# Optimization experiments

Hardware: AMD Instinct MI355X
Metric: run time of the kernel (lower is better)

Reference implementation:

```python
import jax, jax.numpy as jnp
import numpy as np

# Model constants (match init_kwargs)
DIM = 1024
INTER = 1024
E = 32          # n_routed_experts
K = 4           # n_activated_experts
G = 8           # n_expert_groups
LG = 4          # n_limited_groups
ROUTE_SCALE = 1.0
CAP_FACTOR = 1.25
B, S = 4, 2048


def setup_inputs() -> dict:
    key = jax.random.key(0)
    ks = jax.random.split(key, 9)
    sd = DIM ** -0.5
    si = INTER ** -0.5
    x = jax.random.normal(ks[0], (B, S, DIM), jnp.float32)
    wg = jax.random.normal(ks[1], (E, DIM), jnp.float32) * sd          # gate weight [E, dim]
    w1 = jax.random.normal(ks[2], (E, DIM, INTER), jnp.float32) * sd   # stacked expert w1
    w3 = jax.random.normal(ks[3], (E, DIM, INTER), jnp.float32) * sd   # stacked expert w3
    w2 = jax.random.normal(ks[4], (E, INTER, DIM), jnp.float32) * si   # stacked expert w2
    sw1 = jax.random.normal(ks[5], (DIM, INTER), jnp.float32) * sd     # shared SwiGLU
    sw3 = jax.random.normal(ks[6], (DIM, INTER), jnp.float32) * sd
    sw2 = jax.random.normal(ks[7], (INTER, DIM), jnp.float32) * si
    return dict(x=x, wg=wg, w1=w1, w2=w2, w3=w3, sw1=sw1, sw2=sw2, sw3=sw3)


def _gate(xf, wg):
    # Group-limited top-k gating (router_noise_std=0, temperature=1.0).
    logits = xf @ wg.T                                  # [N, E]
    scores = jax.nn.softmax(logits, axis=-1)
    sg = scores.reshape(-1, G, E // G)                  # [N, G, E/G]
    group_scores = sg.max(axis=-1)                      # [N, G]
    _, gtop = jax.lax.top_k(group_scores, LG)           # [N, LG]
    keep_g = jnp.sum(jax.nn.one_hot(gtop, G, dtype=jnp.float32), axis=1) > 0  # [N, G]
    masked = jnp.where(keep_g[:, :, None], sg, -jnp.inf).reshape(-1, E)
    _, idx = jax.lax.top_k(masked, K)                   # [N, K]
    w = jnp.take_along_axis(scores, idx, axis=1)        # gather from ORIGINAL scores
    w = w / (w.sum(-1, keepdims=True) + 1e-9) * ROUTE_SCALE
    return w.astype(xf.dtype), idx


def _forward(x, wg, w1, w2, w3, sw1, sw2, sw3):
    shape = x.shape
    xf = x.reshape(-1, DIM)
    N = xf.shape[0]
    cap = max(1, int(CAP_FACTOR * N * K / E))           # per-expert capacity (static)
    w, idx = _gate(xf, wg)

    # --- dispatch with capacity: position of each (token, slot) within its expert,
    # counted in row-major (token-major) order == torch.where order in the original.
    fe = idx.reshape(-1)                                # [N*K] expert ids
    oh = jax.nn.one_hot(fe, E, dtype=jnp.int32)         # [N*K, E]
    pos = (jnp.cumsum(oh, axis=0) * oh).sum(-1) - 1     # rank within expert
    keep = pos < cap
    dest = jnp.where(keep, fe * cap + pos, E * cap)     # dropped -> pad slot
    tok = jnp.arange(N * K, dtype=jnp.int32) // K
    buf_tok = jnp.full((E * cap + 1,), N, jnp.int32).at[dest].set(tok)[:-1]       # [E*cap]
    buf_w = jnp.zeros((E * cap + 1,), x.dtype).at[dest].set(w.reshape(-1))[:-1]   # [E*cap]

    # --- grouped gather-GEMM-scatter (pad row of zeros for empty slots)
    xp = jnp.concatenate([xf, jnp.zeros((1, DIM), x.dtype)], axis=0)
    xe = xp[buf_tok].reshape(E, cap, DIM)
    h = jax.nn.silu(jnp.einsum('ecd,edh->ech', xe, w1)) * jnp.einsum('ecd,edh->ech', xe, w3)
    out = jnp.einsum('ech,ehd->ecd', h, w2) * buf_w.reshape(E, cap, 1)
    y = jnp.zeros((N + 1, DIM), x.dtype).at[buf_tok].add(out.reshape(E * cap, DIM))[:N]

    # --- shared experts (SwiGLU with inter dim == inter_dim via expansion formula)
    z = (jax.nn.silu(xf @ sw1) * (xf @ sw3)) @ sw2
    return (y + z).reshape(shape)


def reference(x, wg, w1, w2, w3, sw1, sw2, sw3):
    return _forward(x, wg, w1, w2, w3, sw1, sw2, sw3)
```

## Files before the change

### kernel.cpp

```cpp
#include <hip/hip_runtime.h>
#include <stdint.h>

#define NTOK 8192
#define CAP  1280
#define NEXP 32

typedef __bf16 bf16x8 __attribute__((ext_vector_type(8)));
typedef float f32x4 __attribute__((ext_vector_type(4)));
typedef unsigned short u16;

__device__ __forceinline__ u16 f2bf(float f) {
  unsigned u = __builtin_bit_cast(unsigned, f);
  u = (u + 0x7fffu + ((u >> 16) & 1u)) >> 16;
  return (u16)u;
}
__device__ __forceinline__ float bf2f(u16 h) {
  return __builtin_bit_cast(float, ((unsigned)h) << 16);
}

__device__ __forceinline__ void gload16(const void* g, void* l) {
  __builtin_amdgcn_global_load_lds(
      (const __attribute__((address_space(1))) void*)g,
      (__attribute__((address_space(3))) void*)l, 16, 0, 0);
}

__global__ __launch_bounds__(256) void conv_x_kernel(const float* __restrict__ in,
                                                     u16* __restrict__ out) {
  int i = blockIdx.x * 256 + threadIdx.x;
  float4 v = reinterpret_cast<const float4*>(in)[i];
  uint2 o;
  o.x = (unsigned)f2bf(v.x) | ((unsigned)f2bf(v.y) << 16);
  o.y = (unsigned)f2bf(v.z) | ((unsigned)f2bf(v.w) << 16);
  reinterpret_cast<uint2*>(out)[i] = o;
}

__global__ __launch_bounds__(256) void tconv_all_kernel(
    const float* __restrict__ w1, const float* __restrict__ w3,
    const float* __restrict__ w2, const float* __restrict__ sw1,
    const float* __restrict__ sw3, const float* __restrict__ sw2,
    u16* __restrict__ w1t, u16* __restrict__ w3t, u16* __restrict__ w2t,
    u16* __restrict__ sw1t, u16* __restrict__ sw3t, u16* __restrict__ sw2t) {
  __shared__ float tile[32][33];
  const int z = blockIdx.z;
  const float* src;
  u16* dst;
  if (z < 32)      { src = w1 + (size_t)z * 1048576;        dst = w1t + (size_t)z * 1048576; }
  else if (z < 64) { src = w3 + (size_t)(z - 32) * 1048576; dst = w3t + (size_t)(z - 32) * 1048576; }
  else if (z < 96) { src = w2 + (size_t)(z - 64) * 1048576; dst = w2t + (size_t)(z - 64) * 1048576; }
  else if (z == 96){ src = sw1; dst = sw1t; }
  else if (z == 97){ src = sw3; dst = sw3t; }
  else             { src = sw2; dst = sw2t; }
  int r0 = blockIdx.x * 32, c0 = blockIdx.y * 32;
  int tid = threadIdx.x;
#pragma unroll
  for (int i = 0; i < 4; ++i) {
    int t = tid + i * 256, r = t >> 5, c = t & 31;
    tile[r][c] = src[(size_t)(r0 + r) * 1024 + (c0 + c)];
  }
  __syncthreads();
#pragma unroll
  for (int i = 0; i < 4; ++i) {
    int t = tid + i * 256, cc = t >> 5, rr = t & 31;
    dst[(size_t)(c0 + cc) * 1024 + (r0 + rr)] = f2bf(tile[rr][cc]);
  }
}

__global__ __launch_bounds__(256) void gate_kernel(const float* __restrict__ x,
                                                   const float* __restrict__ wg,
                                                   int* __restrict__ gidx,
                                                   float* __restrict__ gw) {
  const int t = blockIdx.x;
  __shared__ float xl[1024];
  __shared__ float logits[32];
  const int tid = threadIdx.x;
  reinterpret_cast<float4*>(xl)[tid] = reinterpret_cast<const float4*>(x + (size_t)t * 1024)[tid];
  __syncthreads();
  const int e = tid >> 3, p = tid & 7;
  const float4* wrow = reinterpret_cast<const float4*>(wg + (size_t)e * 1024);
  const float4* xv4 = reinterpret_cast<const float4*>(xl);
  float s = 0.f;
#pragma unroll
  for (int i = 0; i < 32; ++i) {
    int c = p + 8 * i;
    float4 xv = xv4[c];
    float4 wv = wrow[c];
    s += xv.x * wv.x + xv.y * wv.y + xv.z * wv.z + xv.w * wv.w;
  }
  s += __shfl_xor(s, 1);
  s += __shfl_xor(s, 2);
  s += __shfl_xor(s, 4);
  if (p == 0) logits[e] = s;
  __syncthreads();
  if (tid == 0) {
    float m = logits[0];
#pragma unroll
    for (int i = 1; i < 32; ++i) m = fmaxf(m, logits[i]);
    float sum = 0.f;
#pragma unroll
    for (int i = 0; i < 32; ++i) sum += expf(logits[i] - m);
    float gm[8];
#pragma unroll
    for (int g = 0; g < 8; ++g) {
      float v = logits[4 * g];
      v = fmaxf(v, logits[4 * g + 1]);
      v = fmaxf(v, logits[4 * g + 2]);
      v = fmaxf(v, logits[4 * g + 3]);
      gm[g] = v;
    }
    unsigned gkeep = 0;
    for (int it = 0; it < 4; ++it) {
      float best = -3.4e38f; int bg = 0;
#pragma unroll
      for (int g = 0; g < 8; ++g) {
        bool ok = !((gkeep >> g) & 1u);
        if (ok && gm[g] > best) { best = gm[g]; bg = g; }
      }
      gkeep |= 1u << bg;
    }
    unsigned allow = 0;
#pragma unroll
    for (int g = 0; g < 8; ++g)
      if ((gkeep >> g) & 1u) allow |= 0xFu << (4 * g);
    unsigned taken = 0;
    float wsum = 0.f;
    int ids[4]; float wv[4];
    for (int sIt = 0; sIt < 4; ++sIt) {
      float best = -3.4e38f; int be = 0;
#pragma unroll
      for (int i = 0; i < 32; ++i) {
        bool ok = ((allow >> i) & 1u) && !((taken >> i) & 1u);
        float v = logits[i];
        if (ok && v > best) { best = v; be = i; }
      }
      taken |= 1u << be;
      ids[sIt] = be;
      float wq = expf(logits[be] - m) / sum;
      wv[sIt] = wq;
      wsum += wq;
    }
    float inv = 1.f / (wsum + 1e-9f);
#pragma unroll
    for (int sIt = 0; sIt < 4; ++sIt) {
      gidx[t * 4 + sIt] = ids[sIt];
      gw[t * 4 + sIt] = wv[sIt] * inv;
    }
  }
}

__global__ __launch_bounds__(256) void initbuf_kernel(int* __restrict__ bt, float* __restrict__ bw) {
  int i = blockIdx.x * 256 + threadIdx.x;
  if (i < NEXP * CAP) { bt[i] = -1; bw[i] = 0.f; }
}

__global__ __launch_bounds__(1024) void rank_kernel(const int* __restrict__ gidx,
                                                    const float* __restrict__ gw,
                                                    int* __restrict__ buf_tok,
                                                    float* __restrict__ buf_w,
                                                    int* __restrict__ cnt,
                                                    int* __restrict__ tslot) {
  const int e = blockIdx.x;
  const int tid = threadIdx.x, wid = tid >> 6, lane = tid & 63;
  __shared__ int wtot[16];
  int base = 0;
  for (int j0 = 0; j0 < NTOK * 4; j0 += 1024) {
    int j = j0 + tid;
    bool match = (gidx[j] == e);
    unsigned long long mb = __ballot(match);
    if (lane == 0) wtot[wid] = __popcll(mb);
    __syncthreads();
    int woff = 0, btot = 0;
#pragma unroll
    for (int w = 0; w < 16; ++w) {
      int c = wtot[w];
      if (w < wid) woff += c;
      btot += c;
    }
    if (match) {
      int pos = base + woff + __popcll(mb & ((1ull << lane) - 1ull));
      if (pos < CAP) {
        buf_tok[e * CAP + pos] = j >> 2;
        buf_w[e * CAP + pos] = gw[j];
        tslot[j] = e * CAP + pos;
      } else {
        tslot[j] = -1;
      }
    }
    base += btot;
    __syncthreads();
  }
  if (tid == 0) cnt[e] = (base < CAP) ? base : CAP;
}

#define UP_PHASE(M, EXTRA, LAST)                                                                  \
  {                                                                                               \
    bf16x8 a0 = afrag(cur, M, 0);                                                                 \
    bf16x8 a1 = afrag(cur, M, 1);                                                                 \
    EXTRA                                                                                         \
    __builtin_amdgcn_s_barrier();                                                                 \
    __builtin_amdgcn_s_setprio(1);                                                                \
    _Pragma("unroll")                                                                             \
    for (int n = 0; n < 4; ++n) {                                                                 \
      acc1[M][n] = __builtin_amdgcn_mfma_f32_16x16x32_bf16(a0, b1f[n][0], acc1[M][n], 0, 0, 0);   \
      acc1[M][n] = __builtin_amdgcn_mfma_f32_16x16x32_bf16(a1, b1f[n][1], acc1[M][n], 0, 0, 0);   \
      acc3[M][n] = __builtin_amdgcn_mfma_f32_16x16x32_bf16(a0, b3f[n][0], acc3[M][n], 0, 0, 0);   \
      acc3[M][n] = __builtin_amdgcn_mfma_f32_16x16x32_bf16(a1, b3f[n][1], acc3[M][n], 0, 0, 0);   \
    }                                                                                             \
    __builtin_amdgcn_s_setprio(0);                                                                \
    LAST                                                                                          \
    __builtin_amdgcn_s_barrier();                                                                 \
  }

__global__ __launch_bounds__(512) void up8_kernel(const u16* __restrict__ X,
                                                  const u16* __restrict__ w1t,
                                                  const u16* __restrict__ w3t,
                                                  const u16* __restrict__ sw1t,
                                                  const u16* __restrict__ sw3t,
                                                  u16* __restrict__ hs,
                                                  u16* __restrict__ he,
                                                  const int* __restrict__ btok,
                                                  const int* __restrict__ cnt) {
  extern __shared__ __align__(16) u16 lds_raw[];
  const int tid = threadIdx.x, wid = tid >> 6, lane = tid & 63;
  const int bid = blockIdx.x;
  const int xcd = bid & 7, off = bid >> 3;
  bool expert;
  int mt, nt, e = 0;
  const u16 *B1, *B3;
  u16* H;
  if (off < 160) {
    expert = true;
    int id = xcd * 160 + off;
    e = id / 40;
    int r = id % 40;
    mt = r % 5;
    nt = r / 5;
    if (mt * 256 >= cnt[e]) return;
    B1 = w1t + ((size_t)e << 20);
    B3 = w3t + ((size_t)e << 20);
    H = he + (size_t)(e * CAP + mt * 256) * 1024;
  } else {
    expert = false;
    int id = xcd * 32 + (off - 160);
    mt = id % 32;
    nt = id / 32;
    B1 = sw1t;
    B3 = sw3t;
    H = hs + (size_t)mt * 256 * 1024;
  }
  const int wr = wid >> 1, wc = wid & 1;
  const int fr = lane & 15, fw = lane >> 4;

  const int srow = wid * 8 + (lane >> 3);
  const int swin = (((lane & 7) ^ (srow & 7)) << 3);

  const u16* aP[4];
#pragma unroll
  for (int j = 0; j < 4; ++j) {
    int row = mt * 256 + j * 64 + srow;
    int grow;
    if (expert) {
      int t0 = btok[e * CAP + row];
      grow = (t0 < 0) ? 0 : t0;
    } else {
      grow = row;
    }
    aP[j] = X + (size_t)grow * 1024 + swin;
  }
  const u16* b1P[2];
  const u16* b3P[2];
#pragma unroll
  for (int j = 0; j < 2; ++j) {
    int row = nt * 128 + j * 64 + srow;
    b1P[j] = B1 + (size_t)row * 1024 + swin;
    b3P[j] = B3 + (size_t)row * 1024 + swin;
  }

  auto ldsA  = [&](int b) { return lds_raw + b * 32768; };
  auto ldsB1 = [&](int b) { return lds_raw + b * 32768 + 16384; };
  auto ldsB3 = [&](int b) { return lds_raw + b * 32768 + 24576; };

  auto stageA = [&](int b, int kt) {
    u16* base = ldsA(b) + wid * 512;
#pragma unroll
    for (int j = 0; j < 4; ++j)
      gload16(aP[j] + kt * 64, base + j * 4096);
  };
  auto stageB = [&](int b, int kt) {
    u16* d1 = ldsB1(b) + wid * 512;
    u16* d3 = ldsB3(b) + wid * 512;
#pragma unroll
    for (int j = 0; j < 2; ++j) {
      gload16(b1P[j] + kt * 64, d1 + j * 4096);
      gload16(b3P[j] + kt * 64, d3 + j * 4096);
    }
  };

  auto afrag = [&](int c, int m, int ks) -> bf16x8 {
    int r = wr * 64 + m * 16 + fr;
    int W = ks * 4 + fw;
    return *reinterpret_cast<const bf16x8*>(ldsA(c) + r * 64 + ((W ^ (r & 7)) << 3));
  };
  auto b1frag = [&](int c, int n, int ks) -> bf16x8 {
    int r = wc * 64 + n * 16 + fr;
    int W = ks * 4 + fw;
    return *reinterpret_cast<const bf16x8*>(ldsB1(c) + r * 64 + ((W ^ (r & 7)) << 3));
  };
  auto b3frag = [&](int c, int n, int ks) -> bf16x8 {
    int r = wc * 64 + n * 16 + fr;
    int W = ks * 4 + fw;
    return *reinterpret_cast<const bf16x8*>(ldsB3(c) + r * 64 + ((W ^ (r & 7)) << 3));
  };

  f32x4 acc1[4][4] = {};
  f32x4 acc3[4][4] = {};

  stageA(0, 0);
  stageB(0, 0);
  asm volatile("s_waitcnt vmcnt(0)" ::: "memory");
  __builtin_amdgcn_s_barrier();

  for (int kt = 0; kt < 16; ++kt) {
    const int cur = kt & 1;
    const bool pf = (kt + 1 < 16);
    bf16x8 b1f[4][2], b3f[4][2];
#pragma unroll
    for (int n = 0; n < 4; ++n) {
      b1f[n][0] = b1frag(cur, n, 0);
      b1f[n][1] = b1frag(cur, n, 1);
      b3f[n][0] = b3frag(cur, n, 0);
      b3f[n][1] = b3frag(cur, n, 1);
    }
    UP_PHASE(0, if (pf) stageA(cur ^ 1, kt + 1);, )
    UP_PHASE(1, if (pf) stageB(cur ^ 1, kt + 1);, )
    UP_PHASE(2, , )
    UP_PHASE(3, , asm volatile("s_waitcnt vmcnt(0)" ::: "memory");)
  }

  const int col0 = nt * 128 + wc * 64;
  const int row0 = wr * 64 + fw * 4;
#pragma unroll
  for (int m = 0; m < 4; ++m)
#pragma unroll
    for (int n = 0; n < 4; ++n)
#pragma unroll
      for (int ri = 0; ri < 4; ++ri) {
        int row = row0 + m * 16 + ri;
        int col = col0 + n * 16 + fr;
        float v1 = acc1[m][n][ri];
        float h = (v1 / (1.f + __expf(-v1))) * acc3[m][n][ri];
        H[(size_t)row * 1024 + col] = f2bf(h);
      }
}

__global__ __launch_bounds__(512) void down8_kernel(const u16* __restrict__ hs,
                                                    const u16* __restrict__ he,
                                                    const u16* __restrict__ sB,
                                                    const u16* __restrict__ eB,
                                                    float* __restrict__ Out,
                                                    u16* __restrict__ OutB,
                                                    const float* __restrict__ bw,
                                                    const int* __restrict__ cnt) {
  extern __shared__ __align__(16) u16 lds_raw[];
  const int tid = threadIdx.x, wid = tid >> 6, lane = tid & 63;
  const int bid = blockIdx.x;
  const int xcd = bid & 7, off = bid >> 3;
  bool expert;
  int mt, nt, e = 0;
  const u16 *Asrc, *Bsrc;
  if (off < 80) {
    expert = true;
    int id = xcd * 80 + off;
    e = id / 20;
    int r = id % 20;
    mt = r % 5;
    nt = r / 5;
    if (mt * 256 >= cnt[e]) return;
    Asrc = he + (size_t)e * CAP * 1024;
    Bsrc = eB + ((size_t)e << 20);
  } else {
    expert = false;
    int id = xcd * 16 + (off - 80);
    mt = id % 32;
    nt = id / 32;
    Asrc = hs;
    Bsrc = sB;
  }
  const int wr = wid >> 2, wc = wid & 3;

  const int srow = wid * 8 + (lane >> 3);
  const int sslot = lane & 7;
  const int swin = ((sslot ^ (srow & 7)) << 3);
  const u16* aS = Asrc + (size_t)(mt * 256 + srow) * 1024 + swin;
  const u16* bS = Bsrc + (size_t)(nt * 256 + srow) * 1024 + swin;

  auto ldsA = [&](int b) { return lds_raw + b * 32768; };
  auto ldsB = [&](int b) { return lds_raw + b * 32768 + 16384; };

  auto stageA = [&](int b, int kt) {
    u16* base = ldsA(b);
#pragma unroll
    for (int j = 0; j < 4; ++j)
      gload16(aS + (size_t)j * 64 * 1024 + kt * 64, base + (j * 64 + wid * 8) * 64);
  };
  auto stageB = [&](int b, int kt) {
    u16* base = ldsB(b);
#pragma unroll
    for (int j = 0; j < 4; ++j)
      gload16(bS + (size_t)j * 64 * 1024 + kt * 64, base + (j * 64 + wid * 8) * 64);
  };

  const int fr = lane & 15, fw = lane >> 4;
  auto Afrag = [&](int cur, int m, int ks) -> bf16x8 {
    int r = wr * 128 + m * 16 + fr;
    int W = ks * 4 + fw;
    return *reinterpret_cast<const bf16x8*>(ldsA(cur) + r * 64 + ((W ^ (r & 7)) << 3));
  };
  auto Bfrag = [&](int cur, int n, int ks) -> bf16x8 {
    int r = wc * 64 + n * 16 + fr;
    int W = ks * 4 + fw;
    return *reinterpret_cast<const bf16x8*>(ldsB(cur) + r * 64 + ((W ^ (r & 7)) << 3));
  };

  f32x4 acc[8][4] = {};

  stageA(0, 0);
  stageB(0, 0);
  asm volatile("s_waitcnt vmcnt(0)" ::: "memory");
  __builtin_amdgcn_s_barrier();

  for (int kt = 0; kt < 16; ++kt) {
    const int cur = kt & 1;
    const bool pf = (kt + 1 < 16);
    bf16x8 bfr[4][2];
#pragma unroll
    for (int n = 0; n < 4; ++n) {
      bfr[n][0] = Bfrag(cur, n, 0);
      bfr[n][1] = Bfrag(cur, n, 1);
    }
    {
      bf16x8 a00 = Afrag(cur, 0, 0), a01 = Afrag(cur, 0, 1);
      bf16x8 a10 = Afrag(cur, 1, 0), a11 = Afrag(cur, 1, 1);
      if (pf) stageA(cur ^ 1, kt + 1);
      __builtin_amdgcn_s_barrier();
      __builtin_amdgcn_s_setprio(1);
#pragma unroll
      for (int n = 0; n < 4; ++n) {
        acc[0][n] = __builtin_amdgcn_mfma_f32_16x16x32_bf16(a00, bfr[n][0], acc[0][n], 0, 0, 0);
        acc[0][n] = __builtin_amdgcn_mfma_f32_16x16x32_bf16(a01, bfr[n][1], acc[0][n], 0, 0, 0);
        acc[1][n] = __builtin_amdgcn_mfma_f32_16x16x32_bf16(a10, bfr[n][0], acc[1][n], 0, 0, 0);
        acc[1][n] = __builtin_amdgcn_mfma_f32_16x16x32_bf16(a11, bfr[n][1], acc[1][n], 0, 0, 0);
      }
      __builtin_amdgcn_s_setprio(0);
      __builtin_amdgcn_s_barrier();
    }
    {
      bf16x8 a00 = Afrag(cur, 2, 0), a01 = Afrag(cur, 2, 1);
      bf16x8 a10 = Afrag(cur, 3, 0), a11 = Afrag(cur, 3, 1);
      if (pf) stageB(cur ^ 1, kt + 1);
      __builtin_amdgcn_s_barrier();
      __builtin_amdgcn_s_setprio(1);
#pragma unroll
      for (int n = 0; n < 4; ++n) {
        acc[2][n] = __builtin_amdgcn_mfma_f32_16x16x32_bf16(a00, bfr[n][0], acc[2][n], 0, 0, 0);
        acc[2][n] = __builtin_amdgcn_mfma_f32_16x16x32_bf16(a01, bfr[n][1], acc[2][n], 0, 0, 0);
        acc[3][n] = __builtin_amdgcn_mfma_f32_16x16x32_bf16(a10, bfr[n][0], acc[3][n], 0, 0, 0);
        acc[3][n] = __builtin_amdgcn_mfma_f32_16x16x32_bf16(a11, bfr[n][1], acc[3][n], 0, 0, 0);
      }
      __builtin_amdgcn_s_setprio(0);
      __builtin_amdgcn_s_barrier();
    }
    {
      bf16x8 a00 = Afrag(cur, 4, 0), a01 = Afrag(cur, 4, 1);
      bf16x8 a10 = Afrag(cur, 5, 0), a11 = Afrag(cur, 5, 1);
      __builtin_amdgcn_s_barrier();
      __builtin_amdgcn_s_setprio(1);
#pragma unroll
      for (int n = 0; n < 4; ++n) {
        acc[4][n] = __builtin_amdgcn_mfma_f32_16x16x32_bf16(a00, bfr[n][0], acc[4][n], 0, 0, 0);
        acc[4][n] = __builtin_amdgcn_mfma_f32_16x16x32_bf16(a01, bfr[n][1], acc[4][n], 0, 0, 0);
        acc[5][n] = __builtin_amdgcn_mfma_f32_16x16x32_bf16(a10, bfr[n][0], acc[5][n], 0, 0, 0);
        acc[5][n] = __builtin_amdgcn_mfma_f32_16x16x32_bf16(a11, bfr[n][1], acc[5][n], 0, 0, 0);
      }
      __builtin_amdgcn_s_setprio(0);
      __builtin_amdgcn_s_barrier();
    }
    {
      bf16x8 a00 = Afrag(cur, 6, 0), a01 = Afrag(cur, 6, 1);
      bf16x8 a10 = Afrag(cur, 7, 0), a11 = Afrag(cur, 7, 1);
      __builtin_amdgcn_s_barrier();
      __builtin_amdgcn_s_setprio(1);
#pragma unroll
      for (int n = 0; n < 4; ++n) {
        acc[6][n] = __builtin_amdgcn_mfma_f32_16x16x32_bf16(a00, bfr[n][0], acc[6][n], 0, 0, 0);
        acc[6][n] = __builtin_amdgcn_mfma_f32_16x16x32_bf16(a01, bfr[n][1], acc[6][n], 0, 0, 0);
        acc[7][n] = __builtin_amdgcn_mfma_f32_16x16x32_bf16(a10, bfr[n][0], acc[7][n], 0, 0, 0);
        acc[7][n] = __builtin_amdgcn_mfma_f32_16x16x32_bf16(a11, bfr[n][1], acc[7][n], 0, 0, 0);
      }
      __builtin_amdgcn_s_setprio(0);
      asm volatile("s_waitcnt vmcnt(0)" ::: "memory");
      __builtin_amdgcn_s_barrier();
    }
  }

  const int orow0 = mt * 256 + wr * 128 + fw * 4;
  const int ocol0 = nt * 256 + wc * 64;
  if (expert) {
#pragma unroll
    for (int m = 0; m < 8; ++m)
#pragma unroll
      for (int ri = 0; ri < 4; ++ri) {
        int row = orow0 + m * 16 + ri;
        int slot = e * CAP + row;
        float wgt = bw[slot];
#pragma unroll
        for (int n = 0; n < 4; ++n)
          OutB[(size_t)slot * 1024 + ocol0 + n * 16 + fr] = f2bf(acc[m][n][ri] * wgt);
      }
  } else {
#pragma unroll
    for (int m = 0; m < 8; ++m)
#pragma unroll
      for (int ri = 0; ri < 4; ++ri) {
        int row = orow0 + m * 16 + ri;
#pragma unroll
        for (int n = 0; n < 4; ++n)
          Out[(size_t)row * 1024 + ocol0 + n * 16 + fr] = acc[m][n][ri];
      }
  }
}

__global__ __launch_bounds__(256) void combine_kernel(const u16* __restrict__ oe,
                                                      const int* __restrict__ tslot,
                                                      float* __restrict__ out) {
  const int t = blockIdx.x;
  const int c = threadIdx.x;
  int s0 = tslot[t * 4 + 0], s1 = tslot[t * 4 + 1];
  int s2 = tslot[t * 4 + 2], s3 = tslot[t * 4 + 3];
  float4 v = reinterpret_cast<float4*>(out + (size_t)t * 1024)[c];
  auto addsl = [&](int s) {
    if (s >= 0) {
      uint2 q = reinterpret_cast<const uint2*>(oe + (size_t)s * 1024)[c];
      v.x += bf2f((u16)(q.x & 0xffff));
      v.y += bf2f((u16)(q.x >> 16));
      v.z += bf2f((u16)(q.y & 0xffff));
      v.w += bf2f((u16)(q.y >> 16));
    }
  };
  addsl(s0); addsl(s1); addsl(s2); addsl(s3);
  reinterpret_cast<float4*>(out + (size_t)t * 1024)[c] = v;
}

extern "C" void kernel_launch(void* const* d_in, const int* in_sizes, int n_in,
                              void* d_out, int out_size, void* d_ws, size_t ws_size,
                              hipStream_t stream) {
  const float* x   = (const float*)d_in[0];
  const float* wg  = (const float*)d_in[1];
  const float* w1  = (const float*)d_in[2];
  const float* w2  = (const float*)d_in[3];
  const float* w3  = (const float*)d_in[4];
  const float* sw1 = (const float*)d_in[5];
  const float* sw2 = (const float*)d_in[6];
  const float* sw3 = (const float*)d_in[7];
  float* out = (float*)d_out;

  char* p = (char*)d_ws;
  auto alloc = [&](size_t bytes) {
    char* q = p;
    p += (bytes + 255) & ~(size_t)255;
    return q;
  };
  u16* xb   = (u16*)alloc((size_t)NTOK * 1024 * 2);
  u16* w1t  = (u16*)alloc((size_t)NEXP * 1024 * 1024 * 2);
  u16* w3t  = (u16*)alloc((size_t)NEXP * 1024 * 1024 * 2);
  u16* w2t  = (u16*)alloc((size_t)NEXP * 1024 * 1024 * 2);
  u16* sw1t = (u16*)alloc((size_t)1024 * 1024 * 2);
  u16* sw3t = (u16*)alloc((size_t)1024 * 1024 * 2);
  u16* sw2t = (u16*)alloc((size_t)1024 * 1024 * 2);
  u16* hs   = (u16*)alloc((size_t)NTOK * 1024 * 2);
  u16* he   = (u16*)alloc((size_t)NEXP * CAP * 1024 * 2);
  int*   gidx = (int*)alloc((size_t)NTOK * 4 * 4);
  float* gww  = (float*)alloc((size_t)NTOK * 4 * 4);
  int*   btok = (int*)alloc((size_t)NEXP * CAP * 4);
  float* bww  = (float*)alloc((size_t)NEXP * CAP * 4);
  int*   cnt  = (int*)alloc((size_t)NEXP * 4);
  int*   tslot= (int*)alloc((size_t)NTOK * 4 * 4);
  u16* oe = w1t;

  conv_x_kernel<<<NTOK * 1024 / 1024, 256, 0, stream>>>(x, xb);
  tconv_all_kernel<<<dim3(32, 32, 99), 256, 0, stream>>>(w1, w3, w2, sw1, sw3, sw2,
                                                         w1t, w3t, w2t, sw1t, sw3t, sw2t);
  gate_kernel<<<NTOK, 256, 0, stream>>>(x, wg, gidx, gww);
  initbuf_kernel<<<(NEXP * CAP + 255) / 256, 256, 0, stream>>>(btok, bww);
  rank_kernel<<<NEXP, 1024, 0, stream>>>(gidx, gww, btok, bww, cnt, tslot);
  up8_kernel<<<1536, 512, 131072, stream>>>(xb, w1t, w3t, sw1t, sw3t, hs, he, btok, cnt);
  down8_kernel<<<768, 512, 131072, stream>>>(hs, he, sw2t, w2t, out, oe, bww, cnt);
  combine_kernel<<<NTOK, 256, 0, stream>>>(oe, tslot, out);
}
```

Measured before the change: 549.0 us.

## Restructure up-projection kernel with 4-stage K pipeline and split w1/w3 waves

Rewrites the up8 kernel main loop: K tiles shrink to 32 with a 4-deep LDS ring buffer and vmcnt-based waits, replacing the double-buffered 64-wide K loop. The wave layout changes to 2x4, where half the waves compute the w1 product and half the w3 product over 128 rows each, and results are exchanged through LDS for the SiLU epilogue. The aim is deeper latency hiding and fewer LDS fragment reloads per MFMA. The cost is an extra LDS round-trip and barrier in the epilogue, and more barriers per K step.

```diff
diff --git a/kernel.cpp b/kernel.cpp
--- a/kernel.cpp
+++ b/kernel.cpp
@@ -191,24 +191,30 @@
   if (tid == 0) cnt[e] = (base < CAP) ? base : CAP;
 }
 
-#define UP_PHASE(M, EXTRA, LAST)                                                                  \
-  {                                                                                               \
-    bf16x8 a0 = afrag(cur, M, 0);                                                                 \
-    bf16x8 a1 = afrag(cur, M, 1);                                                                 \
-    EXTRA                                                                                         \
-    __builtin_amdgcn_s_barrier();                                                                 \
-    __builtin_amdgcn_s_setprio(1);                                                                \
-    _Pragma("unroll")                                                                             \
-    for (int n = 0; n < 4; ++n) {                                                                 \
-      acc1[M][n] = __builtin_amdgcn_mfma_f32_16x16x32_bf16(a0, b1f[n][0], acc1[M][n], 0, 0, 0);   \
-      acc1[M][n] = __builtin_amdgcn_mfma_f32_16x16x32_bf16(a1, b1f[n][1], acc1[M][n], 0, 0, 0);   \
-      acc3[M][n] = __builtin_amdgcn_mfma_f32_16x16x32_bf16(a0, b3f[n][0], acc3[M][n], 0, 0, 0);   \
-      acc3[M][n] = __builtin_amdgcn_mfma_f32_16x16x32_bf16(a1, b3f[n][1], acc3[M][n], 0, 0, 0);   \
-    }                                                                                             \
-    __builtin_amdgcn_s_setprio(0);                                                                \
-    LAST                                                                                          \
-    __builtin_amdgcn_s_barrier();                                                                 \
-  }
+#define UPPH(S, STAGE_EXPR, WAIT_STMT)                                           \
+  {                                                                              \
+    const u16* aB = aRd + (S) * 16384;                                           \
+    const u16* bB = bRd + (S) * 16384;                                           \
+    bf16x8 av[8], bv[4];                                                         \
+    _Pragma("unroll") for (int m = 0; m < 8; ++m)                                \
+        av[m] = *reinterpret_cast<const bf16x8*>(aB + m * 512);                  \
+    _Pragma("unroll") for (int n = 0; n < 4; ++n)                                \
+        bv[n] = *reinterpret_cast<const bf16x8*>(bB + n * 512);                  \
+    STAGE_EXPR;                                                                  \
+    WAIT_STMT;                                                                   \
+    __builtin_amdgcn_s_barrier();                                                \
+    __builtin_amdgcn_s_setprio(1);                                               \
+    _Pragma("unroll") for (int m = 0; m < 8; ++m)                                \
+      _Pragma("unroll") for (int n = 0; n < 4; ++n)                              \
+        acc[m][n] = __builtin_amdgcn_mfma_f32_16x16x32_bf16(av[m], bv[n],        \
+                                                            acc[m][n], 0, 0, 0);\
+    __builtin_amdgcn_s_setprio(0);                                               \
+    __builtin_amdgcn_s_barrier();                                                \
+  }
+
+#define VM8 asm volatile("s_waitcnt vmcnt(8)" ::: "memory")
+#define VM4 asm volatile("s_waitcnt vmcnt(4)" ::: "memory")
+#define VM0 asm volatile("s_waitcnt vmcnt(0)" ::: "memory")
 
 __global__ __launch_bounds__(512) void up8_kernel(const u16* __restrict__ X,
                                                   const u16* __restrict__ w1t,
@@ -247,16 +253,17 @@
     B3 = sw3t;
     H = hs + (size_t)mt * 256 * 1024;
   }
-  const int wr = wid >> 1, wc = wid & 1;
+  const int wr = wid >> 2, wc = wid & 3;
   const int fr = lane & 15, fw = lane >> 4;
 
-  const int srow = wid * 8 + (lane >> 3);
-  const int swin = (((lane & 7) ^ (srow & 7)) << 3);
-
-  const u16* aP[4];
-#pragma unroll
-  for (int j = 0; j < 4; ++j) {
-    int row = mt * 256 + j * 64 + srow;
+  const int srow = tid >> 2;
+  const int slot = tid & 3;
+  const int sw = ((slot ^ (srow & 3)) << 3);
+
+  const u16* aP[2];
+#pragma unroll
+  for (int j = 0; j < 2; ++j) {
+    int row = mt * 256 + j * 128 + srow;
     int grow;
     if (expert) {
       int t0 = btok[e * CAP + row];
@@ -264,92 +271,76 @@
     } else {
       grow = row;
     }
-    aP[j] = X + (size_t)grow * 1024 + swin;
-  }
-  const u16* b1P[2];
-  const u16* b3P[2];
-#pragma unroll
-  for (int j = 0; j < 2; ++j) {
-    int row = nt * 128 + j * 64 + srow;
-    b1P[j] = B1 + (size_t)row * 1024 + swin;
-    b3P[j] = B3 + (size_t)row * 1024 + swin;
-  }
-
-  auto ldsA  = [&](int b) { return lds_raw + b * 32768; };
-  auto ldsB1 = [&](int b) { return lds_raw + b * 32768 + 16384; };
-  auto ldsB3 = [&](int b) { return lds_raw + b * 32768 + 24576; };
-
-  auto stageA = [&](int b, int kt) {
-    u16* base = ldsA(b) + wid * 512;
-#pragma unroll
-    for (int j = 0; j < 4; ++j)
-      gload16(aP[j] + kt * 64, base + j * 4096);
-  };
-  auto stageB = [&](int b, int kt) {
-    u16* d1 = ldsB1(b) + wid * 512;
-    u16* d3 = ldsB3(b) + wid * 512;
-#pragma unroll
-    for (int j = 0; j < 2; ++j) {
-      gload16(b1P[j] + kt * 64, d1 + j * 4096);
-      gload16(b3P[j] + kt * 64, d3 + j * 4096);
-    }
-  };
-
-  auto afrag = [&](int c, int m, int ks) -> bf16x8 {
-    int r = wr * 64 + m * 16 + fr;
-    int W = ks * 4 + fw;
-    return *reinterpret_cast<const bf16x8*>(ldsA(c) + r * 64 + ((W ^ (r & 7)) << 3));
-  };
-  auto b1frag = [&](int c, int n, int ks) -> bf16x8 {
-    int r = wc * 64 + n * 16 + fr;
-    int W = ks * 4 + fw;
-    return *reinterpret_cast<const bf16x8*>(ldsB1(c) + r * 64 + ((W ^ (r & 7)) << 3));
-  };
-  auto b3frag = [&](int c, int n, int ks) -> bf16x8 {
-    int r = wc * 64 + n * 16 + fr;
-    int W = ks * 4 + fw;
-    return *reinterpret_cast<const bf16x8*>(ldsB3(c) + r * 64 + ((W ^ (r & 7)) << 3));
-  };
-
-  f32x4 acc1[4][4] = {};
-  f32x4 acc3[4][4] = {};
-
-  stageA(0, 0);
-  stageB(0, 0);
-  asm volatile("s_waitcnt vmcnt(0)" ::: "memory");
+    aP[j] = X + (size_t)grow * 1024 + sw;
+  }
+  const u16* bP[2];
+  bP[0] = B1 + (size_t)(nt * 128 + srow) * 1024 + sw;
+  bP[1] = B3 + (size_t)(nt * 128 + srow) * 1024 + sw;
+
+  const int sdst = wid * 512;
+
+  auto stage = [&](int c) {
+    u16* dA = lds_raw + (c & 3) * 16384 + sdst;
+    u16* dB = dA + 8192;
+    const int g = c * 32;
+    gload16(aP[0] + g, dA);
+    gload16(aP[1] + g, dA + 4096);
+    gload16(bP[0] + g, dB);
+    gload16(bP[1] + g, dB + 4096);
+  };
+
+  const int swz = ((fw ^ (fr & 3)) << 3);
+  const u16* aRd = lds_raw + (wr * 128 + fr) * 32 + swz;
+  const u16* bRd = lds_raw + 8192 + (wc * 64 + fr) * 32 + swz;
+
+  f32x4 acc[8][4] = {};
+
+  stage(0);
+  stage(1);
+  stage(2);
+  VM8;
   __builtin_amdgcn_s_barrier();
 
-  for (int kt = 0; kt < 16; ++kt) {
-    const int cur = kt & 1;
-    const bool pf = (kt + 1 < 16);
-    bf16x8 b1f[4][2], b3f[4][2];
-#pragma unroll
-    for (int n = 0; n < 4; ++n) {
-      b1f[n][0] = b1frag(cur, n, 0);
-      b1f[n][1] = b1frag(cur, n, 1);
-      b3f[n][0] = b3frag(cur, n, 0);
-      b3f[n][1] = b3frag(cur, n, 1);
-    }
-    UP_PHASE(0, if (pf) stageA(cur ^ 1, kt + 1);, )
-    UP_PHASE(1, if (pf) stageB(cur ^ 1, kt + 1);, )
-    UP_PHASE(2, , )
-    UP_PHASE(3, , asm volatile("s_waitcnt vmcnt(0)" ::: "memory");)
-  }
-
-  const int col0 = nt * 128 + wc * 64;
-  const int row0 = wr * 64 + fw * 4;
-#pragma unroll
-  for (int m = 0; m < 4; ++m)
-#pragma unroll
-    for (int n = 0; n < 4; ++n)
-#pragma unroll
-      for (int ri = 0; ri < 4; ++ri) {
-        int row = row0 + m * 16 + ri;
-        int col = col0 + n * 16 + fr;
-        float v1 = acc1[m][n][ri];
-        float h = (v1 / (1.f + __expf(-v1))) * acc3[m][n][ri];
-        H[(size_t)row * 1024 + col] = f2bf(h);
-      }
+  for (int t = 0; t < 7; ++t) {
+    const int p0 = t * 4;
+    UPPH(0, stage(p0 + 3), VM8)
+    UPPH(1, stage(p0 + 4), VM8)
+    UPPH(2, stage(p0 + 5), VM8)
+    UPPH(3, stage(p0 + 6), VM8)
+  }
+  UPPH(0, stage(31), VM8)
+  UPPH(1, (void)0, VM4)
+  UPPH(2, (void)0, VM0)
+  UPPH(3, (void)0, (void)0)
+
+  float* lf = reinterpret_cast<float*>(lds_raw);
+  if (wc >= 2) {
+    float* dst = lf + (wr * 2 + (wc - 2)) * 8192 + lane;
+#pragma unroll
+    for (int m = 0; m < 8; ++m)
+#pragma unroll
+      for (int n = 0; n < 4; ++n)
+#pragma unroll
+        for (int ri = 0; ri < 4; ++ri)
+          dst[(m * 16 + n * 4 + ri) * 64] = acc[m][n][ri];
+  }
+  __syncthreads();
+  if (wc < 2) {
+    const float* src = lf + (wr * 2 + wc) * 8192 + lane;
+    const int row0 = wr * 128 + fw * 4;
+    const int col0 = nt * 128 + wc * 64;
+#pragma unroll
+    for (int m = 0; m < 8; ++m)
+#pragma unroll
+      for (int n = 0; n < 4; ++n)
+#pragma unroll
+        for (int ri = 0; ri < 4; ++ri) {
+          float v1 = acc[m][n][ri];
+          float v3 = src[(m * 16 + n * 4 + ri) * 64];
+          float h = (v1 / (1.f + __expf(-v1))) * v3;
+          H[(size_t)(row0 + m * 16 + ri) * 1024 + col0 + n * 16 + fr] = f2bf(h);
+        }
+  }
 }
 
 __global__ __launch_bounds__(512) void down8_kernel(const u16* __restrict__ hs,
```

After: 593.2 us. +8.0%, slower.
